# Kernel optimization log

Measured on AMD Instinct MI355X. Metric: run time of the kernel, lower is better.

The kernel has to match this reference:

```python
import jax, jax.numpy as jnp
import numpy as np

EPS_LN = 1e-6


def _ln(x):
    m = jnp.mean(x, axis=-1, keepdims=True)
    v = jnp.mean((x - m) ** 2, axis=-1, keepdims=True)
    return (x - m) * jax.lax.rsqrt(v + EPS_LN)


def _rope(q, cos, sin):
    # q: [B,S,H,D]; cos/sin: [S, D//2]; rotate interleaved pairs
    q2 = q.reshape(q.shape[:-1] + (-1, 2))
    a, b = q2[..., 0], q2[..., 1]
    c = cos[None, :, None, :]
    s = sin[None, :, None, :]
    return jnp.stack([a * c - b * s, a * s + b * c], axis=-1).reshape(q.shape)


def _attn(q, k, v):
    # q:[B,Sq,H,D] k,v:[B,Sk,H,D] -> [B,Sq,H,D]; flash default scale 1/sqrt(D)
    D = q.shape[-1]
    scores = jnp.einsum('bqhd,bkhd->bhqk', q, k) / jnp.sqrt(jnp.asarray(D, q.dtype))
    p = jax.nn.softmax(scores, axis=-1)
    return jnp.einsum('bhqk,bkhd->bqhd', p, v)


def setup_inputs() -> dict:
    key = jax.random.key(0)
    C, H, S, T, B = 2048, 16, 1024, 256, 4
    Dh = C // H
    F = int(C * 4)
    L, Ly = B * S, B * T
    ks = jax.random.split(key, 24)

    def w(k, shape):
        return (jax.random.normal(k, shape, dtype=jnp.float32) * 0.02)

    # RoPE angle table: positions 0..S-1 with standard inverse frequencies
    inv_freq = 1.0 / (10000.0 ** (np.arange(0, Dh, 2, dtype=np.float32) / Dh))
    freqs = jnp.asarray(np.arange(S, dtype=np.float32)[:, None] * inv_freq[None, :])

    inp = {
        'x': jax.random.normal(ks[0], (L, C), dtype=jnp.float32),
        'y': jax.random.normal(ks[1], (Ly, C), dtype=jnp.float32),
        't': jax.random.normal(ks[2], (L, 6 * C), dtype=jnp.float32),
        'freqs': freqs,
        'scale_shift_table': jax.random.normal(ks[3], (6, C), dtype=jnp.float32) / (C ** 0.5),
        'Wq_s': w(ks[4], (C, C)), 'bq_s': jnp.zeros((C,), jnp.float32),
        'Wk_s': w(ks[5], (C, C)), 'bk_s': jnp.zeros((C,), jnp.float32),
        'Wv_s': w(ks[6], (C, C)), 'bv_s': jnp.zeros((C,), jnp.float32),
        'Wo_s': w(ks[7], (C, C)), 'bo_s': jnp.zeros((C,), jnp.float32),
        'Wq_c': w(ks[8], (C, C)), 'bq_c': jnp.zeros((C,), jnp.float32),
        'Wk_c': w(ks[9], (C, C)), 'bk_c': jnp.zeros((C,), jnp.float32),
        'Wv_c': w(ks[10], (C, C)), 'bv_c': jnp.zeros((C,), jnp.float32),
        'Wo_c': w(ks[11], (C, C)), 'bo_c': jnp.zeros((C,), jnp.float32),
        'W_fc1': w(ks[12], (F, C)), 'b_fc1': jnp.zeros((F,), jnp.float32),
        'W_fc2': w(ks[13], (C, F)), 'b_fc2': jnp.zeros((C,), jnp.float32),
        'seq_len': S,
        'txt_len': T,
    }
    return inp


def reference(x, y, t, freqs, scale_shift_table,
              Wq_s, bq_s, Wk_s, bk_s, Wv_s, bv_s, Wo_s, bo_s,
              Wq_c, bq_c, Wk_c, bk_c, Wv_c, bv_c, Wo_c, bo_c,
              W_fc1, b_fc1, W_fc2, b_fc2, seq_len, txt_len):
    L, C = x.shape
    Dh = 2 * freqs.shape[1]
    H = C // Dh
    B = L // seq_len
    cos, sin = jnp.cos(freqs), jnp.sin(freqs)

    # per-token AdaLN params (B here == total tokens in torch code)
    mods = scale_shift_table[None] + t.reshape(L, 6, C)
    shift_msa, scale_msa, gate_msa, shift_mlp, scale_mlp, gate_mlp = (
        mods[:, i, :] for i in range(6))

    # ---- self attention (AdaLN modulate + RoPE) ----
    xm = _ln(x) * (1.0 + scale_msa) + shift_msa
    q = (xm @ Wq_s.T + bq_s).reshape(B, seq_len, H, Dh)
    k = (xm @ Wk_s.T + bk_s).reshape(B, seq_len, H, Dh)
    v = (xm @ Wv_s.T + bv_s).reshape(B, seq_len, H, Dh)
    q = _rope(q, cos, sin)
    k = _rope(k, cos, sin)
    a = _attn(q, k, v).reshape(L, C)
    x = x + gate_msa * (a @ Wo_s.T + bo_s)

    # ---- cross attention (no norm/modulation/gate, no RoPE) ----
    q = (x @ Wq_c.T + bq_c).reshape(B, seq_len, H, Dh)
    k = (y @ Wk_c.T + bk_c).reshape(B, txt_len, H, Dh)
    v = (y @ Wv_c.T + bv_c).reshape(B, txt_len, H, Dh)
    a = _attn(q, k, v).reshape(L, C)
    x = x + (a @ Wo_c.T + bo_c)

    # ---- MLP with AdaLN modulate + gate ----
    xm = _ln(x) * (1.0 + scale_mlp) + shift_mlp
    h = jax.nn.gelu(xm @ W_fc1.T + b_fc1, approximate=True)
    x = x + gate_mlp * (h @ W_fc2.T + b_fc2)
    return x
```

## Files before the change

### kernel.cpp

```cpp
#include <hip/hip_runtime.h>
#include <stdint.h>

#define C_DIM 2048
#define H_NUM 16
#define DH    128
#define S_LEN 1024
#define T_LEN 256
#define B_SZ  4
#define L_ROWS 4096
#define LY_ROWS 1024
#define F_DIM 8192

typedef __attribute__((ext_vector_type(4))) float f32x4;
typedef __attribute__((ext_vector_type(8))) __bf16 bf16x8;
typedef __attribute__((ext_vector_type(4))) unsigned short us4;
typedef __attribute__((ext_vector_type(8))) unsigned short us8;
typedef unsigned short u16;

__device__ __forceinline__ u16 f2bf(float f) {
  union { float f; uint32_t u; } v; v.f = f;
  uint32_t r = v.u + 0x7FFFu + ((v.u >> 16) & 1u);
  return (u16)(r >> 16);
}
__device__ __forceinline__ float bf2f(u16 h) {
  union { uint32_t u; float f; } v; v.u = ((uint32_t)h) << 16;
  return v.f;
}

typedef __attribute__((address_space(1))) void gvoid;
typedef __attribute__((address_space(3))) void lvoid;
__device__ __forceinline__ void gl_lds16(const void* g, void* l) {
  __builtin_amdgcn_global_load_lds((gvoid*)g, (lvoid*)l, 16, 0, 0);
}

template<int N> __device__ __forceinline__ void wait_vmcnt() {
  if constexpr (N == 0) asm volatile("s_waitcnt vmcnt(0)" ::: "memory");
  else if constexpr (N == 4) asm volatile("s_waitcnt vmcnt(4)" ::: "memory");
  else if constexpr (N == 5) asm volatile("s_waitcnt vmcnt(5)" ::: "memory");
  else if constexpr (N == 6) asm volatile("s_waitcnt vmcnt(6)" ::: "memory");
}
__device__ __forceinline__ void barrier_raw() {
  asm volatile("s_barrier" ::: "memory");
}
__device__ __forceinline__ void lgkm0_pin() {
  asm volatile("s_waitcnt lgkmcnt(0)" ::: "memory");
  __builtin_amdgcn_sched_barrier(0);
}

__device__ __forceinline__ float gelu_fast(float val) {
  float z = 0.7978845608f * (val + 0.044715f * val * val * val);
  float e = __expf(2.f * z);
  float th = 1.f - 2.f / (e + 1.f);
  return 0.5f * val * (1.f + th);
}

__global__ void k_cvt(const float* __restrict__ src, u16* __restrict__ dst, int n) {
  int i = (blockIdx.x * blockDim.x + threadIdx.x) * 4;
  int stride = gridDim.x * blockDim.x * 4;
  for (; i < n; i += stride) {
    float4 v = *(const float4*)(src + i);
    us4 o;
    o[0] = f2bf(v.x); o[1] = f2bf(v.y); o[2] = f2bf(v.z); o[3] = f2bf(v.w);
    *(us4*)(dst + i) = o;
  }
}

__global__ void k_cvt8(const float* __restrict__ s0, const float* __restrict__ s1,
                       const float* __restrict__ s2, const float* __restrict__ s3,
                       const float* __restrict__ s4, const float* __restrict__ s5,
                       const float* __restrict__ s6, const float* __restrict__ s7,
                       u16* __restrict__ dst) {
  const int PER = C_DIM * C_DIM;
  int i = (blockIdx.x * blockDim.x + threadIdx.x) * 4;
  int stride = gridDim.x * blockDim.x * 4;
  int total = PER * 8;
  for (; i < total; i += stride) {
    int t = i >> 22;
    const float* s;
    switch (t) {
      case 0: s = s0; break; case 1: s = s1; break;
      case 2: s = s2; break; case 3: s = s3; break;
      case 4: s = s4; break; case 5: s = s5; break;
      case 6: s = s6; break; default: s = s7; break;
    }
    float4 v = *(const float4*)(s + (i & (PER - 1)));
    us4 o;
    o[0] = f2bf(v.x); o[1] = f2bf(v.y); o[2] = f2bf(v.z); o[3] = f2bf(v.w);
    *(us4*)(dst + i) = o;
  }
}

__global__ void k_cvt2(const float* __restrict__ s0, const float* __restrict__ s1,
                       u16* __restrict__ dst) {
  const int PER = F_DIM * C_DIM;
  int i = (blockIdx.x * blockDim.x + threadIdx.x) * 4;
  int stride = gridDim.x * blockDim.x * 4;
  int total = PER * 2;
  for (; i < total; i += stride) {
    const float* s = (i >> 24) ? s1 : s0;
    float4 v = *(const float4*)(s + (i & (PER - 1)));
    us4 o;
    o[0] = f2bf(v.x); o[1] = f2bf(v.y); o[2] = f2bf(v.z); o[3] = f2bf(v.w);
    *(us4*)(dst + i) = o;
  }
}

template<int INBF>
__global__ __launch_bounds__(256)
void k_modln(const void* __restrict__ xin, const float* __restrict__ t,
             const float* __restrict__ tab, u16* __restrict__ out,
             int scale_idx, int shift_idx) {
  int row = blockIdx.x;
  int tid = threadIdx.x;
  int c0 = tid * 8;
  float v[8];
  if constexpr (INBF) {
    us8 a = *(const us8*)((const u16*)xin + (size_t)row * C_DIM + c0);
#pragma unroll
    for (int j = 0; j < 8; ++j) v[j] = bf2f(a[j]);
  } else {
    const float* xr = (const float*)xin + (size_t)row * C_DIM;
    float4 a = *(const float4*)(xr + c0);
    float4 b = *(const float4*)(xr + c0 + 4);
    v[0] = a.x; v[1] = a.y; v[2] = a.z; v[3] = a.w;
    v[4] = b.x; v[5] = b.y; v[6] = b.z; v[7] = b.w;
  }
  float s = 0.f, ss = 0.f;
#pragma unroll
  for (int j = 0; j < 8; ++j) { s += v[j]; ss += v[j] * v[j]; }
#pragma unroll
  for (int m = 1; m < 64; m <<= 1) { s += __shfl_xor(s, m); ss += __shfl_xor(ss, m); }
  __shared__ float red[8];
  int wid = tid >> 6;
  if ((tid & 63) == 0) { red[wid * 2] = s; red[wid * 2 + 1] = ss; }
  __syncthreads();
  s  = red[0] + red[2] + red[4] + red[6];
  ss = red[1] + red[3] + red[5] + red[7];
  float mean = s * (1.f / C_DIM);
  float var  = ss * (1.f / C_DIM) - mean * mean;
  float rstd = rsqrtf(var + 1e-6f);
  const float* trow = t + (size_t)row * (6 * C_DIM);
  const float* tsc = trow + scale_idx * C_DIM + c0;
  const float* tsh = trow + shift_idx * C_DIM + c0;
  const float* gsc = tab + scale_idx * C_DIM + c0;
  const float* gsh = tab + shift_idx * C_DIM + c0;
  us8 o;
#pragma unroll
  for (int j = 0; j < 8; ++j) {
    float scv = 1.f + gsc[j] + tsc[j];
    float shv = gsh[j] + tsh[j];
    o[j] = f2bf((v[j] - mean) * rstd * scv + shv);
  }
  *(us8*)(out + (size_t)row * C_DIM + c0) = o;
}

template<int EPI>
__global__ __launch_bounds__(512, 2)
void k_gemm5(const u16* __restrict__ A, const u16* __restrict__ W,
             const float* __restrict__ bias0,
             u16* __restrict__ o0, int out_ld,
             int M, int N, int K, int lda, int ldw, int nbx) {
  __shared__ __align__(16) u16 lds[65536];

  int tid = threadIdx.x;
  int nwg = gridDim.x;
  int q8 = nwg >> 3, r8 = nwg & 7;
  int xcd = blockIdx.x & 7, local = blockIdx.x >> 3;
  int wgid = (xcd < r8 ? xcd * (q8 + 1) : r8 * (q8 + 1) + (xcd - r8) * q8) + local;
  int bx = wgid % nbx, by = wgid / nbx;
  int m0 = by * 256, n0 = bx * 256;

  int wid = tid >> 6, lane = tid & 63;
  int wm = wid >> 2, wn = wid & 3;
  int lr = lane & 15, lg = lane >> 4;
  int xorslot = lr & 7;
  int bcol = (wn & 1) * 64;

  int srow = tid >> 3;
  int scol = ((tid ^ (tid >> 3)) & 7) * 8;

  auto stA = [&](int buf, int h, int kt) {
    u16* dst = lds + (buf * 2 + h) * 8192 + tid * 8;
#pragma unroll
    for (int call = 0; call < 2; ++call) {
      int grow = m0 + h * 128 + call * 64 + srow;
      gl_lds16(A + (size_t)grow * lda + kt * 64 + scol, dst + call * 4096);
    }
  };
  auto stB = [&](int buf, int h, int kt) {
    u16* dst = lds + 32768 + (buf * 2 + h) * 8192 + tid * 8;
#pragma unroll
    for (int call = 0; call < 2; ++call) {
      int grow = n0 + h * 128 + call * 64 + srow;
      gl_lds16(W + (size_t)grow * ldw + kt * 64 + scol, dst + call * 4096);
    }
  };

  f32x4 zero4 = {0.f, 0.f, 0.f, 0.f};
  f32x4 acc[8][4];
#pragma unroll
  for (int m = 0; m < 8; ++m)
#pragma unroll
    for (int n = 0; n < 4; ++n) acc[m][n] = zero4;

  int NT = K >> 6, NJ = NT >> 1;
  stA(0, 0, 0); stA(0, 1, 0); stB(0, 0, 0); stB(0, 1, 0);
  stB(1, 0, 1); stA(1, 0, 1);
  wait_vmcnt<4>();
  barrier_raw();

  for (int j = 0; j < NJ; ++j) {
    bool nlast = (j + 1 < NJ);
    int t1 = 2 * j + 1, t2 = 2 * j + 2, t3 = 2 * j + 3;
#pragma unroll
    for (int buf = 0; buf < 2; ++buf) {
      const u16* Ah = lds + (buf * 2 + wm) * 8192;
      const u16* Bh = lds + 32768 + (buf * 2 + (wn >> 1)) * 8192;
      bf16x8 aR[4][2], b0[2][2], b1[2][2];

#pragma unroll
      for (int m = 0; m < 4; ++m) {
        int r = m * 16 + lr;
#pragma unroll
        for (int kk = 0; kk < 2; ++kk)
          aR[m][kk] = *(const bf16x8*)(Ah + r * 64 + (((kk << 2) | lg) ^ xorslot) * 8);
      }
#pragma unroll
      for (int n = 0; n < 2; ++n) {
        int r = bcol + n * 16 + lr;
#pragma unroll
        for (int kk = 0; kk < 2; ++kk)
          b0[n][kk] = *(const bf16x8*)(Bh + r * 64 + (((kk << 2) | lg) ^ xorslot) * 8);
      }
      if (buf == 0) stA(1, 1, t1);
      else if (nlast) stA(0, 1, t2);
      barrier_raw();
      lgkm0_pin();
      __builtin_amdgcn_s_setprio(1);
#pragma unroll
      for (int kk = 0; kk < 2; ++kk)
#pragma unroll
        for (int m = 0; m < 4; ++m)
#pragma unroll
          for (int n = 0; n < 2; ++n)
            acc[m][n] = __builtin_amdgcn_mfma_f32_16x16x32_bf16(aR[m][kk], b0[n][kk], acc[m][n], 0, 0, 0);
      __builtin_amdgcn_s_setprio(0);
      barrier_raw();

#pragma unroll
      for (int n = 0; n < 2; ++n) {
        int r = bcol + 32 + n * 16 + lr;
#pragma unroll
        for (int kk = 0; kk < 2; ++kk)
          b1[n][kk] = *(const bf16x8*)(Bh + r * 64 + (((kk << 2) | lg) ^ xorslot) * 8);
      }
      if (buf == 0) stB(1, 1, t1);
      else if (nlast) stB(0, 1, t2);
      barrier_raw();
      lgkm0_pin();
      __builtin_amdgcn_s_setprio(1);
#pragma unroll
      for (int kk = 0; kk < 2; ++kk)
#pragma unroll
        for (int m = 0; m < 4; ++m)
#pragma unroll
          for (int n = 0; n < 2; ++n)
            acc[m][2 + n] = __builtin_amdgcn_mfma_f32_16x16x32_bf16(aR[m][kk], b1[n][kk], acc[m][2 + n], 0, 0, 0);
      __builtin_amdgcn_s_setprio(0);
      barrier_raw();

#pragma unroll
      for (int m = 0; m < 4; ++m) {
        int r = 64 + m * 16 + lr;
#pragma unroll
        for (int kk = 0; kk < 2; ++kk)
          aR[m][kk] = *(const bf16x8*)(Ah + r * 64 + (((kk << 2) | lg) ^ xorslot) * 8);
      }
      if (nlast) { if (buf == 0) stB(0, 0, t2); else stB(1, 0, t3); }
      barrier_raw();
      lgkm0_pin();
      __builtin_amdgcn_s_setprio(1);
#pragma unroll
      for (int kk = 0; kk < 2; ++kk)
#pragma unroll
        for (int m = 0; m < 4; ++m)
#pragma unroll
          for (int n = 0; n < 2; ++n)
            acc[4 + m][2 + n] = __builtin_amdgcn_mfma_f32_16x16x32_bf16(aR[m][kk], b1[n][kk], acc[4 + m][2 + n], 0, 0, 0);
      __builtin_amdgcn_s_setprio(0);
      barrier_raw();

      if (nlast) { if (buf == 0) stA(0, 0, t2); else stA(1, 0, t3); }
      barrier_raw();
      __builtin_amdgcn_s_setprio(1);
#pragma unroll
      for (int kk = 0; kk < 2; ++kk)
#pragma unroll
        for (int m = 0; m < 4; ++m)
#pragma unroll
          for (int n = 0; n < 2; ++n)
            acc[4 + m][n] = __builtin_amdgcn_mfma_f32_16x16x32_bf16(aR[m][kk], b0[n][kk], acc[4 + m][n], 0, 0, 0);
      __builtin_amdgcn_s_setprio(0);
      if (nlast) wait_vmcnt<4>(); else wait_vmcnt<0>();
      barrier_raw();
    }
  }

#pragma unroll
  for (int mf = 0; mf < 8; ++mf) {
    int row0 = m0 + wm * 128 + mf * 16 + lg * 4;
#pragma unroll
    for (int nf = 0; nf < 4; ++nf) {
      int col = n0 + wn * 64 + nf * 16 + lr;
      float bv = bias0[col];
#pragma unroll
      for (int r = 0; r < 4; ++r)
        o0[(size_t)(row0 + r) * out_ld + col] = f2bf(gelu_fast(acc[mf][nf][r] + bv));
    }
  }
}

template<int BM, int EPI>
__global__ __launch_bounds__(512, 2)
void k_gemm3(const u16* __restrict__ A, const u16* __restrict__ W,
             const float* __restrict__ bias0, const float* __restrict__ bias1,
             const float* __restrict__ bias2,
             u16* __restrict__ o0, u16* __restrict__ o1, u16* __restrict__ o2,
             int sec_shift, int out_ld,
             float* __restrict__ outF, const float* __restrict__ resid,
             const float* __restrict__ gate_t, const float* __restrict__ gate_tab,
             int M, int N, int K, int lda, int ldw, int nbx) {
  constexpr int HTA = (BM / 2) * 64;
  constexpr int HTB = 128 * 64;
  constexpr int ACALLS = BM / 128;
  constexpr int QM = BM / 64;
  constexpr int MFR = BM / 32;
  constexpr int VMN = 4 + ACALLS;
  constexpr int BOFF = 4 * HTA;
  __shared__ __align__(16) u16 lds[BOFF + 4 * HTB];

  int tid = threadIdx.x;
  int nwg = gridDim.x;
  int q8 = nwg >> 3, r8 = nwg & 7;
  int xcd = blockIdx.x & 7, local = blockIdx.x >> 3;
  int wgid = (xcd < r8 ? xcd * (q8 + 1) : r8 * (q8 + 1) + (xcd - r8) * q8) + local;
  int bx = wgid % nbx, by = wgid / nbx;
  int m0 = by * BM, n0 = bx * 256;

  int wid = tid >> 6, lane = tid & 63;
  int wm = wid >> 2, wn = wid & 3;
  int lr = lane & 15, lg = lane >> 4;
  int xorslot = lr & 7;
  int bcol = (wn & 1) * 64;

  int srow = tid >> 3;
  int scol = ((tid ^ (tid >> 3)) & 7) * 8;

  auto stA = [&](int h, int kt2) {
    int pt = kt2 & 1;
    u16* dst = lds + (pt * 2 + h) * HTA + tid * 8;
#pragma unroll
    for (int call = 0; call < ACALLS; ++call) {
      int grow = m0 + h * (BM / 2) + call * 64 + srow;
      gl_lds16(A + (size_t)grow * lda + kt2 * 64 + scol, dst + call * 4096);
    }
  };
  auto stB = [&](int h, int kt2) {
    int pt = kt2 & 1;
    u16* dst = lds + BOFF + (pt * 2 + h) * HTB + tid * 8;
#pragma unroll
    for (int call = 0; call < 2; ++call) {
      int grow = n0 + h * 128 + call * 64 + srow;
      gl_lds16(W + (size_t)grow * ldw + kt2 * 64 + scol, dst + call * 4096);
    }
  };

  f32x4 zero4 = {0.f, 0.f, 0.f, 0.f};
  f32x4 acc[MFR][4];
#pragma unroll
  for (int m = 0; m < MFR; ++m)
#pragma unroll
    for (int n = 0; n < 4; ++n) acc[m][n] = zero4;

  int NT2 = K >> 6;
  stA(0, 0); stA(1, 0); stB(0, 0); stB(1, 0);
  stB(0, 1); stB(1, 1); stA(0, 1);
  wait_vmcnt<VMN>();
  barrier_raw();

  for (int kt = 0; kt < NT2; ++kt) {
    int p = kt & 1;
    const u16* Ah = lds + (p * 2 + wm) * HTA;
    const u16* Bh = lds + BOFF + (p * 2 + (wn >> 1)) * HTB;
    bf16x8 aR[QM][2], bR0[2][2], bR1[2][2];
    bool st1 = (kt + 1) < NT2, st2 = (kt + 2) < NT2;

#pragma unroll
    for (int m = 0; m < QM; ++m) {
      int r = m * 16 + lr;
#pragma unroll
      for (int kk = 0; kk < 2; ++kk)
        aR[m][kk] = *(const bf16x8*)(Ah + r * 64 + (((kk << 2) | lg) ^ xorslot) * 8);
    }
#pragma unroll
    for (int n = 0; n < 2; ++n) {
      int r = bcol + n * 16 + lr;
#pragma unroll
      for (int kk = 0; kk < 2; ++kk)
        bR0[n][kk] = *(const bf16x8*)(Bh + r * 64 + (((kk << 2) | lg) ^ xorslot) * 8);
    }
    if (st1) stA(1, kt + 1);
    lgkm0_pin();
    __builtin_amdgcn_s_setprio(1);
#pragma unroll
    for (int kk = 0; kk < 2; ++kk)
#pragma unroll
      for (int m = 0; m < QM; ++m)
#pragma unroll
        for (int n = 0; n < 2; ++n)
          acc[m][n] = __builtin_amdgcn_mfma_f32_16x16x32_bf16(aR[m][kk], bR0[n][kk], acc[m][n], 0, 0, 0);
    __builtin_amdgcn_s_setprio(0);
    barrier_raw();

#pragma unroll
    for (int n = 0; n < 2; ++n) {
      int r = bcol + 32 + n * 16 + lr;
#pragma unroll
      for (int kk = 0; kk < 2; ++kk)
        bR1[n][kk] = *(const bf16x8*)(Bh + r * 64 + (((kk << 2) | lg) ^ xorslot) * 8);
    }
    lgkm0_pin();
    __builtin_amdgcn_s_setprio(1);
#pragma unroll
    for (int kk = 0; kk < 2; ++kk)
#pragma unroll
      for (int m = 0; m < QM; ++m)
#pragma unroll
        for (int n = 0; n < 2; ++n)
          acc[m][2 + n] = __builtin_amdgcn_mfma_f32_16x16x32_bf16(aR[m][kk], bR1[n][kk], acc[m][2 + n], 0, 0, 0);
    __builtin_amdgcn_s_setprio(0);
    barrier_raw();

#pragma unroll
    for (int m = 0; m < QM; ++m) {
      int r = (BM / 4) + m * 16 + lr;
#pragma unroll
      for (int kk = 0; kk < 2; ++kk)
        aR[m][kk] = *(const bf16x8*)(Ah + r * 64 + (((kk << 2) | lg) ^ xorslot) * 8);
    }
    if (st2) { stB(0, kt + 2); stB(1, kt + 2); }
    lgkm0_pin();
    __builtin_amdgcn_s_setprio(1);
#pragma unroll
    for (int kk = 0; kk < 2; ++kk)
#pragma unroll
      for (int m = 0; m < QM; ++m)
#pragma unroll
        for (int n = 0; n < 2; ++n)
          acc[QM + m][2 + n] = __builtin_amdgcn_mfma_f32_16x16x32_bf16(aR[m][kk], bR1[n][kk], acc[QM + m][2 + n], 0, 0, 0);
    __builtin_amdgcn_s_setprio(0);
    barrier_raw();

    if (st2) stA(0, kt + 2);
    __builtin_amdgcn_s_setprio(1);
#pragma unroll
    for (int kk = 0; kk < 2; ++kk)
#pragma unroll
      for (int m = 0; m < QM; ++m)
#pragma unroll
        for (int n = 0; n < 2; ++n)
          acc[QM + m][n] = __builtin_amdgcn_mfma_f32_16x16x32_bf16(aR[m][kk], bR0[n][kk], acc[QM + m][n], 0, 0, 0);
    __builtin_amdgcn_s_setprio(0);
    if (st2) wait_vmcnt<VMN>(); else wait_vmcnt<0>();
    barrier_raw();
  }

#pragma unroll
  for (int mf = 0; mf < MFR; ++mf) {
    int row0 = m0 + wm * (BM / 2) + mf * 16 + lg * 4;
#pragma unroll
    for (int nf = 0; nf < 4; ++nf) {
      int col = n0 + wn * 64 + nf * 16 + lr;
      if constexpr (EPI == 0) {
        int sec = col >> sec_shift;
        const float* bp = sec == 0 ? bias0 : (sec == 1 ? bias1 : bias2);
        u16* op = sec == 0 ? o0 : (sec == 1 ? o1 : o2);
        int cs = col & ((1 << sec_shift) - 1);
        float bv = bp[cs];
#pragma unroll
        for (int r = 0; r < 4; ++r)
          op[(size_t)(row0 + r) * out_ld + cs] = f2bf(acc[mf][nf][r] + bv);
      } else if constexpr (EPI == 6) {
        float bv = bias0[col];
        float gt = gate_tab[col];
#pragma unroll
        for (int r = 0; r < 4; ++r) {
          int row = row0 + r;
          size_t idx = (size_t)row * N + col;
          float g = gt + gate_t[(size_t)row * (6 * C_DIM) + col];
          o0[idx] = f2bf(resid[idx] + g * (acc[mf][nf][r] + bv));
        }
      } else if constexpr (EPI == 7) {
        float bv = bias0[col];
#pragma unroll
        for (int r = 0; r < 4; ++r) {
          size_t idx = (size_t)(row0 + r) * N + col;
          o0[idx] = f2bf(bf2f(o0[idx]) + acc[mf][nf][r] + bv);
        }
      } else if constexpr (EPI == 8) {
        float bv = bias0[col];
        float gt = gate_tab[col];
#pragma unroll
        for (int r = 0; r < 4; ++r) {
          int row = row0 + r;
          size_t idx = (size_t)row * N + col;
          float g = gt + gate_t[(size_t)row * (6 * C_DIM) + col];
          outF[idx] = bf2f(((const u16*)o1)[idx]) + g * (acc[mf][nf][r] + bv);
        }
      } else if constexpr (EPI == 9) {
        int sec = col >> 11;
        int cs = col & 2047;
        const float* bp = sec == 0 ? bias0 : (sec == 1 ? bias1 : bias2);
        float bv = bp[cs];
        if (sec < 2) {
          u16* op = sec == 0 ? o0 : o1;
          int i0 = (cs & (DH - 1)) >> 1;
          bool even = (cs & 1) == 0;
#pragma unroll
          for (int r = 0; r < 4; ++r) {
            float val = acc[mf][nf][r] + bv;
            float pv = __shfl_xor(val, 1);
            int sr = (row0 + r) & (S_LEN - 1);
            float ang = gate_t[sr * (DH / 2) + i0];
            float sn, csn;
            __sincosf(ang, &sn, &csn);
            float outv = even ? (val * csn - pv * sn) : (pv * sn + val * csn);
            op[(size_t)(row0 + r) * out_ld + cs] = f2bf(outv);
          }
        } else {
          int h = cs >> 7, d = cs & (DH - 1);
#pragma unroll
          for (int r = 0; r < 4; ++r) {
            int row = row0 + r;
            int b = row >> 10, kv = row & (S_LEN - 1);
            o2[(((size_t)(b * H_NUM + h) * DH + d) << 10) + kv] =
                f2bf(acc[mf][nf][r] + bv);
          }
        }
      } else {
        int sec = col >> 11;
        int cs = col & 2047;
        float bv = (sec == 0 ? bias0 : bias1)[cs];
        if (sec == 0) {
#pragma unroll
          for (int r = 0; r < 4; ++r)
            o0[(size_t)(row0 + r) * out_ld + cs] = f2bf(acc[mf][nf][r] + bv);
        } else {
          int h = cs >> 7, d = cs & (DH - 1);
#pragma unroll
          for (int r = 0; r < 4; ++r) {
            int row = row0 + r;
            int b = row >> 8, kv = row & (T_LEN - 1);
            o1[(((size_t)(b * H_NUM + h) * DH + d) << 8) + kv] =
                f2bf(acc[mf][nf][r] + bv);
          }
        }
      }
    }
  }
}

__global__ __launch_bounds__(256)
void k_flash(const u16* __restrict__ Q, const u16* __restrict__ K,
             const u16* __restrict__ Vt, u16* __restrict__ O,
             int Lq, int Lkv, float scale2) {
  __shared__ __align__(16) u16 lK[64 * 128];
  __shared__ __align__(16) u16 lV[128 * 64];
  __shared__ __align__(16) u16 lP[4][16 * 72];
  int bh = blockIdx.x, b = bh >> 4, h = bh & 15;
  int tid = threadIdx.x, wid = tid >> 6, lane = tid & 63;
  int lr = lane & 15, lg = lane >> 4;
  int q0 = blockIdx.y * 64 + wid * 16;
  const u16* Qb = Q + ((size_t)(b * Lq) + q0) * C_DIM + h * DH;
  const u16* Kb = K + (size_t)(b * Lkv) * C_DIM + h * DH;
  const u16* Vb = Vt + (size_t)bh * DH * Lkv;

  bf16x8 qf[4];
#pragma unroll
  for (int ks = 0; ks < 4; ++ks)
    qf[ks] = *(const bf16x8*)(Qb + (size_t)lr * C_DIM + ks * 32 + lg * 8);

  f32x4 zero4 = {0.f, 0.f, 0.f, 0.f};
  f32x4 o[8];
#pragma unroll
  for (int n = 0; n < 8; ++n) o[n] = zero4;
  float mrow[4] = {-3.0e38f, -3.0e38f, -3.0e38f, -3.0e38f};
  float lrow[4] = {0.f, 0.f, 0.f, 0.f};

  int nsteps = Lkv >> 6;
  for (int kt = 0; kt < nsteps; ++kt) {
#pragma unroll
    for (int i = 0; i < 4; ++i) {
      int flat = i * 4096 + tid * 16;
      int key = flat >> 8, inner = flat & 255;
      int ksrc = inner ^ ((key & 7) << 4);
      gl_lds16((const char*)Kb + ((size_t)(kt * 64 + key) * C_DIM) * 2 + ksrc, (char*)lK + flat);
      int d = flat >> 7, keyb = flat & 127;
      int vsrc = keyb ^ ((d & 7) << 4);
      gl_lds16((const char*)Vb + ((size_t)d * Lkv) * 2 + kt * 128 + vsrc, (char*)lV + flat);
    }
    __syncthreads();

    f32x4 sc[4];
#pragma unroll
    for (int c = 0; c < 4; ++c) sc[c] = zero4;
#pragma unroll
    for (int c = 0; c < 4; ++c) {
      int key = c * 16 + lr;
#pragma unroll
      for (int ks = 0; ks < 4; ++ks) {
        int off = (ks * 64 + lg * 16) ^ ((key & 7) << 4);
        bf16x8 kf = *(const bf16x8*)((const char*)lK + key * 256 + off);
        sc[c] = __builtin_amdgcn_mfma_f32_16x16x32_bf16(qf[ks], kf, sc[c], 0, 0, 0);
      }
    }
#pragma unroll
    for (int r = 0; r < 4; ++r) {
      float s0 = sc[0][r] * scale2, s1 = sc[1][r] * scale2;
      float s2 = sc[2][r] * scale2, s3 = sc[3][r] * scale2;
      float mx = fmaxf(fmaxf(s0, s1), fmaxf(s2, s3));
#pragma unroll
      for (int m = 1; m < 16; m <<= 1) mx = fmaxf(mx, __shfl_xor(mx, m));
      float mnew = fmaxf(mrow[r], mx);
      float alpha = exp2f(mrow[r] - mnew);
      mrow[r] = mnew;
      float p0 = exp2f(s0 - mnew);
      float p1 = exp2f(s1 - mnew);
      float p2 = exp2f(s2 - mnew);
      float p3 = exp2f(s3 - mnew);
      float psum = p0 + p1 + p2 + p3;
#pragma unroll
      for (int m = 1; m < 16; m <<= 1) psum += __shfl_xor(psum, m);
      lrow[r] = lrow[r] * alpha + psum;
#pragma unroll
      for (int n = 0; n < 8; ++n) o[n][r] *= alpha;
      u16* pr = lP[wid] + (4 * lg + r) * 72;
      pr[lr]      = f2bf(p0);
      pr[16 + lr] = f2bf(p1);
      pr[32 + lr] = f2bf(p2);
      pr[48 + lr] = f2bf(p3);
    }
    asm volatile("s_waitcnt lgkmcnt(0)" ::: "memory");
    __builtin_amdgcn_sched_barrier(0);
#pragma unroll
    for (int half = 0; half < 2; ++half) {
      bf16x8 pf = *(const bf16x8*)(lP[wid] + lr * 72 + half * 32 + lg * 8);
#pragma unroll
      for (int n = 0; n < 8; ++n) {
        int d = n * 16 + lr;
        int off = (half * 64 + lg * 16) ^ ((d & 7) << 4);
        bf16x8 vf = *(const bf16x8*)((const char*)lV + d * 128 + off);
        o[n] = __builtin_amdgcn_mfma_f32_16x16x32_bf16(pf, vf, o[n], 0, 0, 0);
      }
    }
    __syncthreads();
  }

  u16* Ob = O + ((size_t)(b * Lq) + q0) * C_DIM + h * DH;
#pragma unroll
  for (int n = 0; n < 8; ++n) {
    int d = n * 16 + lr;
#pragma unroll
    for (int r = 0; r < 4; ++r) {
      int qr = 4 * lg + r;
      Ob[(size_t)qr * C_DIM + d] = f2bf(o[n][r] / lrow[r]);
    }
  }
}

extern "C" void kernel_launch(void* const* d_in, const int* in_sizes, int n_in,
                              void* d_out, int out_size, void* d_ws, size_t ws_size,
                              hipStream_t stream) {
  const float* x     = (const float*)d_in[0];
  const float* y     = (const float*)d_in[1];
  const float* t     = (const float*)d_in[2];
  const float* freqs = (const float*)d_in[3];
  const float* tab   = (const float*)d_in[4];
  const float* Wq_s = (const float*)d_in[5];
  const float* bq_s = (const float*)d_in[6];
  const float* Wk_s = (const float*)d_in[7];
  const float* bk_s = (const float*)d_in[8];
  const float* Wv_s = (const float*)d_in[9];
  const float* bv_s = (const float*)d_in[10];
  const float* Wo_s = (const float*)d_in[11];
  const float* bo_s = (const float*)d_in[12];
  const float* Wq_c = (const float*)d_in[13];
  const float* bq_c = (const float*)d_in[14];
  const float* Wk_c = (const float*)d_in[15];
  const float* bk_c = (const float*)d_in[16];
  const float* Wv_c = (const float*)d_in[17];
  const float* bv_c = (const float*)d_in[18];
  const float* Wo_c = (const float*)d_in[19];
  const float* bo_c = (const float*)d_in[20];
  const float* W_fc1 = (const float*)d_in[21];
  const float* b_fc1 = (const float*)d_in[22];
  const float* W_fc2 = (const float*)d_in[23];
  const float* b_fc2 = (const float*)d_in[24];

  const size_t SZ_CC  = (size_t)C_DIM * C_DIM * 2;
  const size_t SZ_FC  = (size_t)F_DIM * C_DIM * 2;
  const size_t SZ_LC  = (size_t)L_ROWS * C_DIM * 2;
  const size_t SZ_YC  = (size_t)LY_ROWS * C_DIM * 2;
  char* ws = (char*)d_ws;
  size_t off = 0;
  u16* wq_s = (u16*)(ws + off); off += SZ_CC;
  u16* wk_s = (u16*)(ws + off); off += SZ_CC;
  u16* wv_s = (u16*)(ws + off); off += SZ_CC;
  u16* wo_s = (u16*)(ws + off); off += SZ_CC;
  u16* wq_c = (u16*)(ws + off); off += SZ_CC;
  u16* wk_c = (u16*)(ws + off); off += SZ_CC;
  u16* wv_c = (u16*)(ws + off); off += SZ_CC;
  u16* wo_c = (u16*)(ws + off); off += SZ_CC;
  u16* wfc1 = (u16*)(ws + off); off += SZ_FC;
  u16* wfc2 = (u16*)(ws + off); off += SZ_FC;
  u16* ybf  = (u16*)(ws + off); off += SZ_YC;
  u16* xm   = (u16*)(ws + off); off += SZ_LC;
  u16* qb   = (u16*)(ws + off); off += SZ_LC;
  u16* kb   = (u16*)(ws + off); off += SZ_LC;
  u16* vb   = (u16*)(ws + off); off += SZ_LC;
  u16* ao   = (u16*)(ws + off); off += SZ_LC;
  u16* hbuf = qb;
  u16* x1bf = (u16*)(ws + off); off += SZ_LC;
  u16* kc   = (u16*)(ws + off); off += SZ_YC;
  u16* vc   = (u16*)(ws + off); off += SZ_YC;
  u16* vt   = (u16*)(ws + off); off += SZ_LC;
  u16* vtc  = (u16*)(ws + off); off += SZ_YC;
  if (ws_size < off) return;
  (void)vb; (void)vc;

  k_cvt8<<<4096, 256, 0, stream>>>(Wq_s, Wk_s, Wv_s, Wo_s, Wq_c, Wk_c, Wv_c, Wo_c, wq_s);
  k_cvt2<<<4096, 256, 0, stream>>>(W_fc1, W_fc2, wfc1);
  k_cvt<<<2048, 256, 0, stream>>>(y, ybf, LY_ROWS * C_DIM);

  const float ascale2 = 0.08838834764831845f * 1.44269504f;

  k_modln<0><<<L_ROWS, 256, 0, stream>>>(x, t, tab, xm, 1, 0);
  k_gemm3<128, 9><<<32 * 24, 512, 0, stream>>>(
      xm, wq_s, bq_s, bk_s, bv_s, qb, kb, vt, 11, C_DIM,
      nullptr, nullptr, freqs, nullptr, L_ROWS, 6144, C_DIM, C_DIM, C_DIM, 24);
  k_flash<<<dim3(B_SZ * H_NUM, S_LEN / 64), 256, 0, stream>>>(qb, kb, vt, ao, S_LEN, S_LEN, ascale2);
  k_gemm3<128, 6><<<32 * 8, 512, 0, stream>>>(
      ao, wo_s, bo_s, nullptr, nullptr, x1bf, nullptr, nullptr, 30, C_DIM,
      nullptr, x, t + 2 * C_DIM, tab + 2 * C_DIM, L_ROWS, C_DIM, C_DIM, C_DIM, C_DIM, 8);
  k_gemm3<128, 0><<<32 * 8, 512, 0, stream>>>(
      x1bf, wq_c, bq_c, nullptr, nullptr, qb, nullptr, nullptr, 30, C_DIM,
      nullptr, nullptr, nullptr, nullptr, L_ROWS, C_DIM, C_DIM, C_DIM, C_DIM, 8);
  k_gemm3<128, 10><<<8 * 16, 512, 0, stream>>>(
      ybf, wk_c, bk_c, bv_c, nullptr, kc, vtc, nullptr, 11, C_DIM,
      nullptr, nullptr, nullptr, nullptr, LY_ROWS, 4096, C_DIM, C_DIM, C_DIM, 16);
  k_flash<<<dim3(B_SZ * H_NUM, S_LEN / 64), 256, 0, stream>>>(qb, kc, vtc, ao, S_LEN, T_LEN, ascale2);
  k_gemm3<128, 7><<<32 * 8, 512, 0, stream>>>(
      ao, wo_c, bo_c, nullptr, nullptr, x1bf, nullptr, nullptr, 30, C_DIM,
      nullptr, nullptr, nullptr, nullptr, L_ROWS, C_DIM, C_DIM, C_DIM, C_DIM, 8);
  k_modln<1><<<L_ROWS, 256, 0, stream>>>(x1bf, t, tab, xm, 4, 3);
  k_gemm5<1><<<16 * 32, 512, 0, stream>>>(
      xm, wfc1, b_fc1, hbuf, F_DIM, L_ROWS, F_DIM, C_DIM, C_DIM, C_DIM, 32);
  k_gemm3<128, 8><<<32 * 8, 512, 0, stream>>>(
      hbuf, wfc2, b_fc2, nullptr, nullptr, nullptr, x1bf, nullptr, 30, C_DIM,
      (float*)d_out, nullptr, t + 5 * C_DIM, tab + 5 * C_DIM, L_ROWS, C_DIM, F_DIM, F_DIM, F_DIM, 8);
}
```

Measured before the change: 835.2 us.

## Replace GEMM kernels with single 128x256 K=32 triple-buffered GEMM at higher occupancy

Removes the 256x256 FC1 GEMM and the BM-templated GEMM and replaces both with one kernel. It uses 128x256 tiles and K-steps of 32, keeps A in a three-slot ring and B in two buffers, uses fewer barriers per step, and sets launch bounds to 4 waves per SIMD. The goal is more occupancy and less LDS and register pressure so memory latency is hidden by other workgroups. In exchange each tile gets less operand reuse per load, and the shorter K-steps mean more loop iterations and more synchronisation overhead per unit of work.

```diff
diff --git a/kernel.cpp b/kernel.cpp
--- a/kernel.cpp
+++ b/kernel.cpp
@@ -35,9 +35,7 @@
 
 template<int N> __device__ __forceinline__ void wait_vmcnt() {
   if constexpr (N == 0) asm volatile("s_waitcnt vmcnt(0)" ::: "memory");
-  else if constexpr (N == 4) asm volatile("s_waitcnt vmcnt(4)" ::: "memory");
-  else if constexpr (N == 5) asm volatile("s_waitcnt vmcnt(5)" ::: "memory");
-  else if constexpr (N == 6) asm volatile("s_waitcnt vmcnt(6)" ::: "memory");
+  else if constexpr (N == 3) asm volatile("s_waitcnt vmcnt(3)" ::: "memory");
 }
 __device__ __forceinline__ void barrier_raw() {
   asm volatile("s_barrier" ::: "memory");
@@ -155,174 +153,8 @@
 }
 
 template<int EPI>
-__global__ __launch_bounds__(512, 2)
-void k_gemm5(const u16* __restrict__ A, const u16* __restrict__ W,
-             const float* __restrict__ bias0,
-             u16* __restrict__ o0, int out_ld,
-             int M, int N, int K, int lda, int ldw, int nbx) {
-  __shared__ __align__(16) u16 lds[65536];
-
-  int tid = threadIdx.x;
-  int nwg = gridDim.x;
-  int q8 = nwg >> 3, r8 = nwg & 7;
-  int xcd = blockIdx.x & 7, local = blockIdx.x >> 3;
-  int wgid = (xcd < r8 ? xcd * (q8 + 1) : r8 * (q8 + 1) + (xcd - r8) * q8) + local;
-  int bx = wgid % nbx, by = wgid / nbx;
-  int m0 = by * 256, n0 = bx * 256;
-
-  int wid = tid >> 6, lane = tid & 63;
-  int wm = wid >> 2, wn = wid & 3;
-  int lr = lane & 15, lg = lane >> 4;
-  int xorslot = lr & 7;
-  int bcol = (wn & 1) * 64;
-
-  int srow = tid >> 3;
-  int scol = ((tid ^ (tid >> 3)) & 7) * 8;
-
-  auto stA = [&](int buf, int h, int kt) {
-    u16* dst = lds + (buf * 2 + h) * 8192 + tid * 8;
-#pragma unroll
-    for (int call = 0; call < 2; ++call) {
-      int grow = m0 + h * 128 + call * 64 + srow;
-      gl_lds16(A + (size_t)grow * lda + kt * 64 + scol, dst + call * 4096);
-    }
-  };
-  auto stB = [&](int buf, int h, int kt) {
-    u16* dst = lds + 32768 + (buf * 2 + h) * 8192 + tid * 8;
-#pragma unroll
-    for (int call = 0; call < 2; ++call) {
-      int grow = n0 + h * 128 + call * 64 + srow;
-      gl_lds16(W + (size_t)grow * ldw + kt * 64 + scol, dst + call * 4096);
-    }
-  };
-
-  f32x4 zero4 = {0.f, 0.f, 0.f, 0.f};
-  f32x4 acc[8][4];
-#pragma unroll
-  for (int m = 0; m < 8; ++m)
-#pragma unroll
-    for (int n = 0; n < 4; ++n) acc[m][n] = zero4;
-
-  int NT = K >> 6, NJ = NT >> 1;
-  stA(0, 0, 0); stA(0, 1, 0); stB(0, 0, 0); stB(0, 1, 0);
-  stB(1, 0, 1); stA(1, 0, 1);
-  wait_vmcnt<4>();
-  barrier_raw();
-
-  for (int j = 0; j < NJ; ++j) {
-    bool nlast = (j + 1 < NJ);
-    int t1 = 2 * j + 1, t2 = 2 * j + 2, t3 = 2 * j + 3;
-#pragma unroll
-    for (int buf = 0; buf < 2; ++buf) {
-      const u16* Ah = lds + (buf * 2 + wm) * 8192;
-      const u16* Bh = lds + 32768 + (buf * 2 + (wn >> 1)) * 8192;
-      bf16x8 aR[4][2], b0[2][2], b1[2][2];
-
-#pragma unroll
-      for (int m = 0; m < 4; ++m) {
-        int r = m * 16 + lr;
-#pragma unroll
-        for (int kk = 0; kk < 2; ++kk)
-          aR[m][kk] = *(const bf16x8*)(Ah + r * 64 + (((kk << 2) | lg) ^ xorslot) * 8);
-      }
-#pragma unroll
-      for (int n = 0; n < 2; ++n) {
-        int r = bcol + n * 16 + lr;
-#pragma unroll
-        for (int kk = 0; kk < 2; ++kk)
-          b0[n][kk] = *(const bf16x8*)(Bh + r * 64 + (((kk << 2) | lg) ^ xorslot) * 8);
-      }
-      if (buf == 0) stA(1, 1, t1);
-      else if (nlast) stA(0, 1, t2);
-      barrier_raw();
-      lgkm0_pin();
-      __builtin_amdgcn_s_setprio(1);
-#pragma unroll
-      for (int kk = 0; kk < 2; ++kk)
-#pragma unroll
-        for (int m = 0; m < 4; ++m)
-#pragma unroll
-          for (int n = 0; n < 2; ++n)
-            acc[m][n] = __builtin_amdgcn_mfma_f32_16x16x32_bf16(aR[m][kk], b0[n][kk], acc[m][n], 0, 0, 0);
-      __builtin_amdgcn_s_setprio(0);
-      barrier_raw();
-
-#pragma unroll
-      for (int n = 0; n < 2; ++n) {
-        int r = bcol + 32 + n * 16 + lr;
-#pragma unroll
-        for (int kk = 0; kk < 2; ++kk)
-          b1[n][kk] = *(const bf16x8*)(Bh + r * 64 + (((kk << 2) | lg) ^ xorslot) * 8);
-      }
-      if (buf == 0) stB(1, 1, t1);
-      else if (nlast) stB(0, 1, t2);
-      barrier_raw();
-      lgkm0_pin();
-      __builtin_amdgcn_s_setprio(1);
-#pragma unroll
-      for (int kk = 0; kk < 2; ++kk)
-#pragma unroll
-        for (int m = 0; m < 4; ++m)
-#pragma unroll
-          for (int n = 0; n < 2; ++n)
-            acc[m][2 + n] = __builtin_amdgcn_mfma_f32_16x16x32_bf16(aR[m][kk], b1[n][kk], acc[m][2 + n], 0, 0, 0);
-      __builtin_amdgcn_s_setprio(0);
-      barrier_raw();
-
-#pragma unroll
-      for (int m = 0; m < 4; ++m) {
-        int r = 64 + m * 16 + lr;
-#pragma unroll
-        for (int kk = 0; kk < 2; ++kk)
-          aR[m][kk] = *(const bf16x8*)(Ah + r * 64 + (((kk << 2) | lg) ^ xorslot) * 8);
-      }
-      if (nlast) { if (buf == 0) stB(0, 0, t2); else stB(1, 0, t3); }
-      barrier_raw();
-      lgkm0_pin();
-      __builtin_amdgcn_s_setprio(1);
-#pragma unroll
-      for (int kk = 0; kk < 2; ++kk)
-#pragma unroll
-        for (int m = 0; m < 4; ++m)
-#pragma unroll
-          for (int n = 0; n < 2; ++n)
-            acc[4 + m][2 + n] = __builtin_amdgcn_mfma_f32_16x16x32_bf16(aR[m][kk], b1[n][kk], acc[4 + m][2 + n], 0, 0, 0);
-      __builtin_amdgcn_s_setprio(0);
-      barrier_raw();
-
-      if (nlast) { if (buf == 0) stA(0, 0, t2); else stA(1, 0, t3); }
-      barrier_raw();
-      __builtin_amdgcn_s_setprio(1);
-#pragma unroll
-      for (int kk = 0; kk < 2; ++kk)
-#pragma unroll
-        for (int m = 0; m < 4; ++m)
-#pragma unroll
-          for (int n = 0; n < 2; ++n)
-            acc[4 + m][n] = __builtin_amdgcn_mfma_f32_16x16x32_bf16(aR[m][kk], b0[n][kk], acc[4 + m][n], 0, 0, 0);
-      __builtin_amdgcn_s_setprio(0);
-      if (nlast) wait_vmcnt<4>(); else wait_vmcnt<0>();
-      barrier_raw();
-    }
-  }
-
-#pragma unroll
-  for (int mf = 0; mf < 8; ++mf) {
-    int row0 = m0 + wm * 128 + mf * 16 + lg * 4;
-#pragma unroll
-    for (int nf = 0; nf < 4; ++nf) {
-      int col = n0 + wn * 64 + nf * 16 + lr;
-      float bv = bias0[col];
-#pragma unroll
-      for (int r = 0; r < 4; ++r)
-        o0[(size_t)(row0 + r) * out_ld + col] = f2bf(gelu_fast(acc[mf][nf][r] + bv));
-    }
-  }
-}
-
-template<int BM, int EPI>
-__global__ __launch_bounds__(512, 2)
-void k_gemm3(const u16* __restrict__ A, const u16* __restrict__ W,
+__global__ __launch_bounds__(512, 4)
+void k_gemm6(const u16* __restrict__ A, const u16* __restrict__ W,
              const float* __restrict__ bias0, const float* __restrict__ bias1,
              const float* __restrict__ bias2,
              u16* __restrict__ o0, u16* __restrict__ o1, u16* __restrict__ o2,
@@ -330,14 +162,10 @@
              float* __restrict__ outF, const float* __restrict__ resid,
              const float* __restrict__ gate_t, const float* __restrict__ gate_tab,
              int M, int N, int K, int lda, int ldw, int nbx) {
-  constexpr int HTA = (BM / 2) * 64;
-  constexpr int HTB = 128 * 64;
-  constexpr int ACALLS = BM / 128;
-  constexpr int QM = BM / 64;
-  constexpr int MFR = BM / 32;
-  constexpr int VMN = 4 + ACALLS;
-  constexpr int BOFF = 4 * HTA;
-  __shared__ __align__(16) u16 lds[BOFF + 4 * HTB];
+  constexpr int ASZ = 128 * 32;
+  constexpr int BSZ = 256 * 32;
+  constexpr int BOFF = 3 * ASZ;
+  __shared__ __align__(16) u16 lds[BOFF + 2 * BSZ];
 
   int tid = threadIdx.x;
   int nwg = gridDim.x;
@@ -345,151 +173,107 @@
   int xcd = blockIdx.x & 7, local = blockIdx.x >> 3;
   int wgid = (xcd < r8 ? xcd * (q8 + 1) : r8 * (q8 + 1) + (xcd - r8) * q8) + local;
   int bx = wgid % nbx, by = wgid / nbx;
-  int m0 = by * BM, n0 = bx * 256;
+  int m0 = by * 128, n0 = bx * 256;
 
   int wid = tid >> 6, lane = tid & 63;
   int wm = wid >> 2, wn = wid & 3;
   int lr = lane & 15, lg = lane >> 4;
-  int xorslot = lr & 7;
-  int bcol = (wn & 1) * 64;
-
-  int srow = tid >> 3;
-  int scol = ((tid ^ (tid >> 3)) & 7) * 8;
-
-  auto stA = [&](int h, int kt2) {
-    int pt = kt2 & 1;
-    u16* dst = lds + (pt * 2 + h) * HTA + tid * 8;
-#pragma unroll
-    for (int call = 0; call < ACALLS; ++call) {
-      int grow = m0 + h * (BM / 2) + call * 64 + srow;
-      gl_lds16(A + (size_t)grow * lda + kt2 * 64 + scol, dst + call * 4096);
-    }
+  int xorslot = lr & 3;
+
+  int srow = tid >> 2;
+  int scol = ((tid ^ (tid >> 2)) & 3) * 8;
+
+  auto stA = [&](int buf, int kt) {
+    gl_lds16(A + (size_t)(m0 + srow) * lda + kt * 32 + scol,
+             lds + buf * ASZ + tid * 8);
   };
-  auto stB = [&](int h, int kt2) {
-    int pt = kt2 & 1;
-    u16* dst = lds + BOFF + (pt * 2 + h) * HTB + tid * 8;
-#pragma unroll
-    for (int call = 0; call < 2; ++call) {
-      int grow = n0 + h * 128 + call * 64 + srow;
-      gl_lds16(W + (size_t)grow * ldw + kt2 * 64 + scol, dst + call * 4096);
+  auto stB = [&](int buf, int kt) {
+    u16* dst = lds + BOFF + buf * BSZ + tid * 8;
+#pragma unroll
+    for (int c = 0; c < 2; ++c) {
+      int grow = n0 + c * 128 + srow;
+      gl_lds16(W + (size_t)grow * ldw + kt * 32 + scol, dst + c * 4096);
     }
   };
 
   f32x4 zero4 = {0.f, 0.f, 0.f, 0.f};
-  f32x4 acc[MFR][4];
-#pragma unroll
-  for (int m = 0; m < MFR; ++m)
+  f32x4 acc[4][4];
+#pragma unroll
+  for (int m = 0; m < 4; ++m)
 #pragma unroll
     for (int n = 0; n < 4; ++n) acc[m][n] = zero4;
 
-  int NT2 = K >> 6;
-  stA(0, 0); stA(1, 0); stB(0, 0); stB(1, 0);
-  stB(0, 1); stB(1, 1); stA(0, 1);
-  wait_vmcnt<VMN>();
+  int NT = K >> 5;
+  stA(0, 0); stB(0, 0);
+  stA(1, 1); stB(1, 1);
+  wait_vmcnt<3>();
   barrier_raw();
 
-  for (int kt = 0; kt < NT2; ++kt) {
-    int p = kt & 1;
-    const u16* Ah = lds + (p * 2 + wm) * HTA;
-    const u16* Bh = lds + BOFF + (p * 2 + (wn >> 1)) * HTB;
-    bf16x8 aR[QM][2], bR0[2][2], bR1[2][2];
-    bool st1 = (kt + 1) < NT2, st2 = (kt + 2) < NT2;
-
-#pragma unroll
-    for (int m = 0; m < QM; ++m) {
+  int a3 = 0;
+  for (int kt = 0; kt < NT; ++kt) {
+    int bp = kt & 1;
+    int a3n = a3 + 2 >= 3 ? a3 - 1 : a3 + 2;
+    const u16* Ah = lds + a3 * ASZ + wm * (64 * 32);
+    const u16* Bh = lds + BOFF + bp * BSZ + wn * (64 * 32);
+    bf16x8 aR[2], bR[4];
+    bool st2 = (kt + 2) < NT;
+
+#pragma unroll
+    for (int m = 0; m < 2; ++m) {
       int r = m * 16 + lr;
-#pragma unroll
-      for (int kk = 0; kk < 2; ++kk)
-        aR[m][kk] = *(const bf16x8*)(Ah + r * 64 + (((kk << 2) | lg) ^ xorslot) * 8);
-    }
-#pragma unroll
-    for (int n = 0; n < 2; ++n) {
-      int r = bcol + n * 16 + lr;
-#pragma unroll
-      for (int kk = 0; kk < 2; ++kk)
-        bR0[n][kk] = *(const bf16x8*)(Bh + r * 64 + (((kk << 2) | lg) ^ xorslot) * 8);
-    }
-    if (st1) stA(1, kt + 1);
+      aR[m] = *(const bf16x8*)(Ah + r * 32 + (lg ^ xorslot) * 8);
+    }
+#pragma unroll
+    for (int n = 0; n < 4; ++n) {
+      int r = n * 16 + lr;
+      bR[n] = *(const bf16x8*)(Bh + r * 32 + (lg ^ xorslot) * 8);
+    }
+    if (st2) stA(a3n, kt + 2);
     lgkm0_pin();
     __builtin_amdgcn_s_setprio(1);
 #pragma unroll
-    for (int kk = 0; kk < 2; ++kk)
-#pragma unroll
-      for (int m = 0; m < QM; ++m)
-#pragma unroll
-        for (int n = 0; n < 2; ++n)
-          acc[m][n] = __builtin_amdgcn_mfma_f32_16x16x32_bf16(aR[m][kk], bR0[n][kk], acc[m][n], 0, 0, 0);
+    for (int m = 0; m < 2; ++m)
+#pragma unroll
+      for (int n = 0; n < 4; ++n)
+        acc[m][n] = __builtin_amdgcn_mfma_f32_16x16x32_bf16(aR[m], bR[n], acc[m][n], 0, 0, 0);
     __builtin_amdgcn_s_setprio(0);
     barrier_raw();
 
 #pragma unroll
-    for (int n = 0; n < 2; ++n) {
-      int r = bcol + 32 + n * 16 + lr;
-#pragma unroll
-      for (int kk = 0; kk < 2; ++kk)
-        bR1[n][kk] = *(const bf16x8*)(Bh + r * 64 + (((kk << 2) | lg) ^ xorslot) * 8);
-    }
+    for (int m = 0; m < 2; ++m) {
+      int r = 32 + m * 16 + lr;
+      aR[m] = *(const bf16x8*)(Ah + r * 32 + (lg ^ xorslot) * 8);
+    }
+    if (st2) stB(bp, kt + 2);
     lgkm0_pin();
     __builtin_amdgcn_s_setprio(1);
 #pragma unroll
-    for (int kk = 0; kk < 2; ++kk)
-#pragma unroll
-      for (int m = 0; m < QM; ++m)
-#pragma unroll
-        for (int n = 0; n < 2; ++n)
-          acc[m][2 + n] = __builtin_amdgcn_mfma_f32_16x16x32_bf16(aR[m][kk], bR1[n][kk], acc[m][2 + n], 0, 0, 0);
+    for (int m = 0; m < 2; ++m)
+#pragma unroll
+      for (int n = 0; n < 4; ++n)
+        acc[2 + m][n] = __builtin_amdgcn_mfma_f32_16x16x32_bf16(aR[m], bR[n], acc[2 + m][n], 0, 0, 0);
     __builtin_amdgcn_s_setprio(0);
+    if (st2) wait_vmcnt<3>(); else wait_vmcnt<0>();
     barrier_raw();
-
-#pragma unroll
-    for (int m = 0; m < QM; ++m) {
-      int r = (BM / 4) + m * 16 + lr;
-#pragma unroll
-      for (int kk = 0; kk < 2; ++kk)
-        aR[m][kk] = *(const bf16x8*)(Ah + r * 64 + (((kk << 2) | lg) ^ xorslot) * 8);
-    }
-    if (st2) { stB(0, kt + 2); stB(1, kt + 2); }
-    lgkm0_pin();
-    __builtin_amdgcn_s_setprio(1);
-#pragma unroll
-    for (int kk = 0; kk < 2; ++kk)
-#pragma unroll
-      for (int m = 0; m < QM; ++m)
-#pragma unroll
-        for (int n = 0; n < 2; ++n)
-          acc[QM + m][2 + n] = __builtin_amdgcn_mfma_f32_16x16x32_bf16(aR[m][kk], bR1[n][kk], acc[QM + m][2 + n], 0, 0, 0);
-    __builtin_amdgcn_s_setprio(0);
-    barrier_raw();
-
-    if (st2) stA(0, kt + 2);
-    __builtin_amdgcn_s_setprio(1);
-#pragma unroll
-    for (int kk = 0; kk < 2; ++kk)
-#pragma unroll
-      for (int m = 0; m < QM; ++m)
-#pragma unroll
-        for (int n = 0; n < 2; ++n)
-          acc[QM + m][n] = __builtin_amdgcn_mfma_f32_16x16x32_bf16(aR[m][kk], bR0[n][kk], acc[QM + m][n], 0, 0, 0);
-    __builtin_amdgcn_s_setprio(0);
-    if (st2) wait_vmcnt<VMN>(); else wait_vmcnt<0>();
-    barrier_raw();
-  }
-
-#pragma unroll
-  for (int mf = 0; mf < MFR; ++mf) {
-    int row0 = m0 + wm * (BM / 2) + mf * 16 + lg * 4;
+    a3 = a3 + 1 >= 3 ? 0 : a3 + 1;
+  }
+
+#pragma unroll
+  for (int mf = 0; mf < 4; ++mf) {
+    int row0 = m0 + wm * 64 + mf * 16 + lg * 4;
 #pragma unroll
     for (int nf = 0; nf < 4; ++nf) {
       int col = n0 + wn * 64 + nf * 16 + lr;
       if constexpr (EPI == 0) {
-        int sec = col >> sec_shift;
-        const float* bp = sec == 0 ? bias0 : (sec == 1 ? bias1 : bias2);
-        u16* op = sec == 0 ? o0 : (sec == 1 ? o1 : o2);
-        int cs = col & ((1 << sec_shift) - 1);
-        float bv = bp[cs];
+        float bv = bias0[col];
 #pragma unroll
         for (int r = 0; r < 4; ++r)
-          op[(size_t)(row0 + r) * out_ld + cs] = f2bf(acc[mf][nf][r] + bv);
+          o0[(size_t)(row0 + r) * out_ld + col] = f2bf(acc[mf][nf][r] + bv);
+      } else if constexpr (EPI == 1) {
+        float bv = bias0[col];
+#pragma unroll
+        for (int r = 0; r < 4; ++r)
+          o0[(size_t)(row0 + r) * out_ld + col] = f2bf(gelu_fast(acc[mf][nf][r] + bv));
       } else if constexpr (EPI == 6) {
         float bv = bias0[col];
         float gt = gate_tab[col];
@@ -520,8 +304,8 @@
       } else if constexpr (EPI == 9) {
         int sec = col >> 11;
         int cs = col & 2047;
-        const float* bp = sec == 0 ? bias0 : (sec == 1 ? bias1 : bias2);
-        float bv = bp[cs];
+        const float* bp2 = sec == 0 ? bias0 : (sec == 1 ? bias1 : bias2);
+        float bv = bp2[cs];
         if (sec < 2) {
           u16* op = sec == 0 ? o0 : o1;
           int i0 = (cs & (DH - 1)) >> 1;
@@ -745,27 +529,28 @@
   const float ascale2 = 0.08838834764831845f * 1.44269504f;
 
   k_modln<0><<<L_ROWS, 256, 0, stream>>>(x, t, tab, xm, 1, 0);
-  k_gemm3<128, 9><<<32 * 24, 512, 0, stream>>>(
+  k_gemm6<9><<<24 * 32, 512, 0, stream>>>(
       xm, wq_s, bq_s, bk_s, bv_s, qb, kb, vt, 11, C_DIM,
       nullptr, nullptr, freqs, nullptr, L_ROWS, 6144, C_DIM, C_DIM, C_DIM, 24);
   k_flash<<<dim3(B_SZ * H_NUM, S_LEN / 64), 256, 0, stream>>>(qb, kb, vt, ao, S_LEN, S_LEN, ascale2);
-  k_gemm3<128, 6><<<32 * 8, 512, 0, stream>>>(
+  k_gemm6<6><<<8 * 32, 512, 0, stream>>>(
       ao, wo_s, bo_s, nullptr, nullptr, x1bf, nullptr, nullptr, 30, C_DIM,
       nullptr, x, t + 2 * C_DIM, tab + 2 * C_DIM, L_ROWS, C_DIM, C_DIM, C_DIM, C_DIM, 8);
-  k_gemm3<128, 0><<<32 * 8, 512, 0, stream>>>(
+  k_gemm6<0><<<8 * 32, 512, 0, stream>>>(
       x1bf, wq_c, bq_c, nullptr, nullptr, qb, nullptr, nullptr, 30, C_DIM,
       nullptr, nullptr, nullptr, nullptr, L_ROWS, C_DIM, C_DIM, C_DIM, C_DIM, 8);
-  k_gemm3<128, 10><<<8 * 16, 512, 0, stream>>>(
+  k_gemm6<10><<<16 * 8, 512, 0, stream>>>(
       ybf, wk_c, bk_c, bv_c, nullptr, kc, vtc, nullptr, 11, C_DIM,
       nullptr, nullptr, nullptr, nullptr, LY_ROWS, 4096, C_DIM, C_DIM, C_DIM, 16);
   k_flash<<<dim3(B_SZ * H_NUM, S_LEN / 64), 256, 0, stream>>>(qb, kc, vtc, ao, S_LEN, T_LEN, ascale2);
-  k_gemm3<128, 7><<<32 * 8, 512, 0, stream>>>(
+  k_gemm6<7><<<8 * 32, 512, 0, stream>>>(
       ao, wo_c, bo_c, nullptr, nullptr, x1bf, nullptr, nullptr, 30, C_DIM,
       nullptr, nullptr, nullptr, nullptr, L_ROWS, C_DIM, C_DIM, C_DIM, C_DIM, 8);
   k_modln<1><<<L_ROWS, 256, 0, stream>>>(x1bf, t, tab, xm, 4, 3);
-  k_gemm5<1><<<16 * 32, 512, 0, stream>>>(
-      xm, wfc1, b_fc1, hbuf, F_DIM, L_ROWS, F_DIM, C_DIM, C_DIM, C_DIM, 32);
-  k_gemm3<128, 8><<<32 * 8, 512, 0, stream>>>(
+  k_gemm6<1><<<32 * 32, 512, 0, stream>>>(
+      xm, wfc1, b_fc1, nullptr, nullptr, hbuf, nullptr, nullptr, 30, F_DIM,
+      nullptr, nullptr, nullptr, nullptr, L_ROWS, F_DIM, C_DIM, C_DIM, C_DIM, 32);
+  k_gemm6<8><<<8 * 32, 512, 0, stream>>>(
       hbuf, wfc2, b_fc2, nullptr, nullptr, nullptr, x1bf, nullptr, 30, C_DIM,
       (float*)d_out, nullptr, t + 5 * C_DIM, tab + 5 * C_DIM, L_ROWS, C_DIM, F_DIM, F_DIM, F_DIM, 8);
 }
```

Result: slower. 926.2 us (+10.9%).
